# Optimization experiments

Measured on AMD Instinct MI355X. Metric: run time of the kernel, lower is better.

The kernel has to match this reference:

```python
import jax, jax.numpy as jnp
import numpy as np

IMG = 512
STRIDE = 16
K = 9
FM = IMG // STRIDE          # 32
N = FM * FM * K             # 9216 anchors
IOU_THR = 0.7
POST_NMS_TOPK = 300
C_FEAT = 512


def _conv(x, w, b, stride=1, padding='SAME'):
    y = jax.lax.conv_general_dilated(x, w, (stride, stride), padding,
                                     dimension_numbers=('NCHW', 'OIHW', 'NCHW'))
    return y + b[None, :, None, None]


def _make_anchors():
    scales = [64.0, 128.0, 256.0]
    ratios = [0.5, 1.0, 2.0]
    wh = np.array([[s * np.sqrt(r), s / np.sqrt(r)] for s in scales for r in ratios],
                  np.float32)                                    # [K,2]
    ctr = (np.arange(FM, dtype=np.float32) + 0.5) * STRIDE
    cy, cx = np.meshgrid(ctr, ctr, indexing='ij')               # [FM,FM]
    c = np.stack([cx, cy], -1)[:, :, None, :]                   # [FM,FM,1,2]
    half = wh[None, None, :, :] / 2.0                           # [1,1,K,2]
    boxes = np.concatenate([c - half, c + half], -1)            # [FM,FM,K,4]
    return boxes.reshape(-1, 4)


def setup_inputs():
    key = jax.random.key(0)
    ks = jax.random.split(key, 5)
    p = lambda k, shp, s: jax.random.normal(k, shp, jnp.float32) * s
    return {
        'input_image': jax.random.normal(ks[0], (1, 3, IMG, IMG), jnp.float32),
        'anchors': jnp.asarray(_make_anchors()),
        'w_bb': p(ks[1], (C_FEAT, 3, STRIDE, STRIDE), 0.05),
        'b_bb': jnp.zeros((C_FEAT,), jnp.float32),
        'w_rpn': p(ks[2], (C_FEAT, C_FEAT, 3, 3), 0.02),
        'b_rpn': jnp.zeros((C_FEAT,), jnp.float32),
        'w_cls': p(ks[3], (2 * K, C_FEAT, 1, 1), 0.01),
        'b_cls': jnp.zeros((2 * K,), jnp.float32),
        'w_box': p(ks[4], (4 * K, C_FEAT, 1, 1), 0.01),
        'b_box': jnp.zeros((4 * K,), jnp.float32),
    }


def _decode_clip(anchors, deltas):
    # apply_delta_to_anchors + clip_boxes
    wa = anchors[:, 2] - anchors[:, 0]
    ha = anchors[:, 3] - anchors[:, 1]
    cxa = anchors[:, 0] + 0.5 * wa
    cya = anchors[:, 1] + 0.5 * ha
    dx, dy = deltas[:, 0], deltas[:, 1]
    dw = jnp.clip(deltas[:, 2], -4.0, 4.0)   # numeric guard on exp
    dh = jnp.clip(deltas[:, 3], -4.0, 4.0)
    cx = cxa + dx * wa
    cy = cya + dy * ha
    w = wa * jnp.exp(dw)
    h = ha * jnp.exp(dh)
    x1 = jnp.maximum(cx - 0.5 * w, 0.0)
    y1 = jnp.maximum(cy - 0.5 * h, 0.0)
    x2 = jnp.minimum(cx + 0.5 * w, IMG - 1.0)
    y2 = jnp.minimum(cy + 0.5 * h, IMG - 1.0)
    return jnp.stack([x1, y1, x2, y2], -1)


def _iou_matrix(b):
    x1, y1, x2, y2 = b[:, 0], b[:, 1], b[:, 2], b[:, 3]
    area = (x2 - x1) * (y2 - y1)
    iw = jnp.clip(jnp.minimum(x2[:, None], x2[None, :]) - jnp.maximum(x1[:, None], x1[None, :]), 0.0)
    ih = jnp.clip(jnp.minimum(y2[:, None], y2[None, :]) - jnp.maximum(y1[:, None], y1[None, :]), 0.0)
    inter = iw * ih
    return inter / (area[:, None] + area[None, :] - inter + 1e-9)


def _nms_keep(boxes_sorted):
    # boxes_sorted: [N,4] in descending score order; greedy hard NMS.
    iou = jax.lax.stop_gradient(_iou_matrix(boxes_sorted))  # [N,N]
    idx = jnp.arange(N)

    def body(i, keep):
        sup = keep[i] & (iou[i] > IOU_THR) & (idx > i)
        return keep & ~sup

    return jax.lax.fori_loop(0, N, body, jnp.ones((N,), bool))


def reference(input_image, anchors, w_bb, b_bb, w_rpn, b_rpn, w_cls, b_cls, w_box, b_box):
    # backbone
    feat = jax.nn.relu(_conv(input_image, w_bb, b_bb, stride=STRIDE, padding='VALID'))  # [1,512,32,32]
    # rpn
    hid = jax.nn.relu(_conv(feat, w_rpn, b_rpn))
    cls = _conv(hid, w_cls, b_cls)   # [1,2K,FM,FM]
    box = _conv(hid, w_box, b_box)   # [1,4K,FM,FM]
    # foreground scores: cls_scores[:, k:, :, :]
    scores = cls[0, K:, :, :].transpose(1, 2, 0).reshape(-1)                    # [N]
    deltas = box[0].reshape(K, 4, FM, FM).transpose(2, 3, 0, 1).reshape(-1, 4)  # [N,4]
    proposals = _decode_clip(anchors, deltas)
    order = jnp.argsort(-scores)
    boxes_s = proposals[order]
    keep = _nms_keep(boxes_s)
    # first 300 kept boxes (score order); fixed shape via stable argsort on keep flag
    sel = jnp.argsort((~keep).astype(jnp.int32), stable=True)[:POST_NMS_TOPK]
    return boxes_s[sel]
```

## Files before the change

kernel.cpp:

```cpp
#include <hip/hip_runtime.h>
#include <stdint.h>

typedef unsigned long long u64;

#define PTOT 1024
#define CF   512
#define NBOX 9216
#define NW   144
#define TOPK 300

__device__ __forceinline__ uint32_t score_key(float s) {
  uint32_t b = __float_as_uint(s);
  uint32_t o = (b & 0x80000000u) ? ~b : (b | 0x80000000u);
  return ~o;
}

#define FMA16() do { \
  acc[0][0] = fmaf(bv.x, av.x, acc[0][0]); \
  acc[0][1] = fmaf(bv.x, av.y, acc[0][1]); \
  acc[0][2] = fmaf(bv.x, av.z, acc[0][2]); \
  acc[0][3] = fmaf(bv.x, av.w, acc[0][3]); \
  acc[1][0] = fmaf(bv.y, av.x, acc[1][0]); \
  acc[1][1] = fmaf(bv.y, av.y, acc[1][1]); \
  acc[1][2] = fmaf(bv.y, av.z, acc[1][2]); \
  acc[1][3] = fmaf(bv.y, av.w, acc[1][3]); \
  acc[2][0] = fmaf(bv.z, av.x, acc[2][0]); \
  acc[2][1] = fmaf(bv.z, av.y, acc[2][1]); \
  acc[2][2] = fmaf(bv.z, av.z, acc[2][2]); \
  acc[2][3] = fmaf(bv.z, av.w, acc[2][3]); \
  acc[3][0] = fmaf(bv.w, av.x, acc[3][0]); \
  acc[3][1] = fmaf(bv.w, av.y, acc[3][1]); \
  acc[3][2] = fmaf(bv.w, av.z, acc[3][2]); \
  acc[3][3] = fmaf(bv.w, av.w, acc[3][3]); \
} while (0)

__global__ __launch_bounds__(256) void k_wt(const float* __restrict__ w_rpn,
                                            const float* __restrict__ w_bb,
                                            float* __restrict__ wT,
                                            float* __restrict__ wT1) {
  __shared__ float T[32][33];
  int bx = blockIdx.x;
  const float* src; float* dst; int K, kb;
  if (bx < 144) { src = w_rpn; dst = wT; K = 4608; kb = bx * 32; }
  else          { src = w_bb;  dst = wT1; K = 768; kb = (bx - 144) * 32; }
  const int cob = blockIdx.y * 32;
  const int tx = threadIdx.x & 31, ty = threadIdx.x >> 5;
#pragma unroll
  for (int r = 0; r < 32; r += 8)
    T[ty + r][tx] = src[(cob + ty + r) * K + kb + tx];
  __syncthreads();
#pragma unroll
  for (int r = 0; r < 32; r += 8)
    dst[(kb + ty + r) * 512 + cob + tx] = T[tx][ty + r];
}

__global__ __launch_bounds__(256) void k_conv1(const float* __restrict__ img,
                                               const float* __restrict__ wT1,
                                               float* __restrict__ featP) {
  __shared__ __align__(16) float As[32][72];
  __shared__ __align__(16) float Bs[32][64];
  const int t = threadIdx.x;
  const int pbase = blockIdx.x * 64;
  const int cobase = blockIdx.y * 64;
  const int z = blockIdx.z;
  const int pg = t & 15, cg = t >> 4;
  const int pp0 = pg * 4, cc0 = cg * 4;
  const int py0 = pbase >> 5;
  float acc[4][4] = {};
  for (int kb = 0; kb < 256; kb += 32) {
    const int ky0 = kb >> 4;
#pragma unroll
    for (int l0 = 0; l0 < 2048; l0 += 256) {
      int l = l0 + t;
      int seg = l >> 9, off = l & 511;
      int py_off = seg >> 1, ky_off = seg & 1;
      int row = (py0 + py_off) * 16 + ky0 + ky_off;
      float v = img[(z * 512 + row) * 512 + off];
      As[ky_off * 16 + (off & 15)][py_off * 32 + (off >> 4)] = v;
    }
#pragma unroll
    for (int it = 0; it < 2; ++it) {
      int idx4 = it * 256 + t;
      int k = idx4 >> 4, co4 = (idx4 & 15) << 2;
      *(float4*)&Bs[k][co4] =
          *(const float4*)&wT1[(z * 256 + kb + k) * 512 + cobase + co4];
    }
    __syncthreads();
#pragma unroll
    for (int kk = 0; kk < 32; ++kk) {
      float4 av = *(const float4*)&As[kk][pp0];
      float4 bv = *(const float4*)&Bs[kk][cc0];
      FMA16();
    }
    __syncthreads();
  }
#pragma unroll
  for (int i = 0; i < 4; ++i) {
    float* o = &featP[((size_t)z * CF + cobase + cc0 + i) * PTOT + pbase + pp0];
    *(float4*)o = make_float4(acc[i][0], acc[i][1], acc[i][2], acc[i][3]);
  }
}

__global__ __launch_bounds__(256) void k_reduce1(const float* __restrict__ featP,
                                                 const float* __restrict__ bias,
                                                 float* __restrict__ feat) {
  int idx4 = blockIdx.x * 256 + threadIdx.x;
  int co = idx4 >> 8;
  const float4* f = (const float4*)featP;
  float4 a = f[idx4];
  float4 b = f[idx4 + 131072];
  float4 c = f[idx4 + 262144];
  float bb = bias[co];
  float4 o;
  o.x = fmaxf(a.x + b.x + c.x + bb, 0.f);
  o.y = fmaxf(a.y + b.y + c.y + bb, 0.f);
  o.z = fmaxf(a.z + b.z + c.z + bb, 0.f);
  o.w = fmaxf(a.w + b.w + c.w + bb, 0.f);
  ((float4*)feat)[idx4] = o;
}

__global__ __launch_bounds__(256) void k_conv2(const float* __restrict__ feat,
                                               const float* __restrict__ wT,
                                               float* __restrict__ hidP,
                                               int ciPerZ) {
  __shared__ __align__(16) float As[8][6][44];
  __shared__ __align__(16) float Bs[72 * 64];
  const int t = threadIdx.x;
  const int pyb = blockIdx.x * 4;
  const int cob = blockIdx.y * 64;
  const int z = blockIdx.z;
  const int cib = z * ciPerZ;
  const int pg = t & 15, cg = t >> 4;
  const int prow = pg >> 2, px0 = (pg & 3) * 8;
  const int co0 = cg * 4;
  float acc[4][8] = {};
  for (int cc = 0; cc < ciPerZ; cc += 8) {
    {
      int idx4 = t;
#pragma unroll
      for (int it = 0; it < 2; ++it, idx4 += 256) {
        if (idx4 < 480) {
          int ci = idx4 / 60;
          int rem = idx4 - ci * 60;
          int row = rem / 10;
          int col4 = (rem - row * 10) << 2;
          int x = col4 - 4;
          int gy = pyb + row - 1;
          float4 v = make_float4(0.f, 0.f, 0.f, 0.f);
          if (x >= 0 && x < 32 && gy >= 0 && gy < 32)
            v = *(const float4*)&feat[(cib + cc + ci) * PTOT + gy * 32 + x];
          *(float4*)&As[ci][row][col4] = v;
        }
      }
    }
    {
      const int kg0 = (cib + cc) * 9;
      int idx4 = t;
#pragma unroll
      for (int it = 0; it < 5; ++it, idx4 += 256) {
        if (idx4 < 1152) {
          int k = idx4 >> 4;
          int co4 = (idx4 & 15) << 2;
          *(float4*)&Bs[k * 64 + co4] =
              *(const float4*)&wT[(kg0 + k) * 512 + cob + co4];
        }
      }
    }
    __syncthreads();
#pragma unroll 1
    for (int ci = 0; ci < 8; ++ci) {
#pragma unroll
      for (int dy = 0; dy < 3; ++dy) {
        const float* Ar = &As[ci][prow + dy][px0];
        float rw[16];
        *(float4*)&rw[0]  = *(const float4*)&Ar[0];
        *(float4*)&rw[4]  = *(const float4*)&Ar[4];
        *(float4*)&rw[8]  = *(const float4*)&Ar[8];
        *(float4*)&rw[12] = *(const float4*)&Ar[12];
#pragma unroll
        for (int dx = 0; dx < 3; ++dx) {
          const float* Bp = &Bs[(ci * 9 + dy * 3 + dx) * 64 + co0];
          float4 b0 = *(const float4*)&Bp[0];
          float bm[4] = {b0.x, b0.y, b0.z, b0.w};
#pragma unroll
          for (int m = 0; m < 4; ++m)
#pragma unroll
            for (int j = 0; j < 8; ++j)
              acc[m][j] = fmaf(rw[3 + dx + j], bm[m], acc[m][j]);
        }
      }
    }
    __syncthreads();
  }
  const int prowg = pyb + prow;
#pragma unroll
  for (int m = 0; m < 4; ++m) {
    int co = cob + co0 + m;
    float* o = &hidP[((size_t)z * CF + co) * PTOT + prowg * 32 + px0];
    *(float4*)&o[0] = make_float4(acc[m][0], acc[m][1], acc[m][2], acc[m][3]);
    *(float4*)&o[4] = make_float4(acc[m][4], acc[m][5], acc[m][6], acc[m][7]);
  }
}

__global__ __launch_bounds__(256) void k_reduce2(const float* __restrict__ hidP,
                                                 const float* __restrict__ bias,
                                                 float* __restrict__ hid_t, int Z) {
  __shared__ float T[64][65];
  const int co0 = blockIdx.x * 64, p0 = blockIdx.y * 64;
  const int t = threadIdx.x;
#pragma unroll
  for (int it = 0; it < 4; ++it) {
    int idx4 = it * 256 + t;
    int co = idx4 >> 4, p4 = (idx4 & 15) << 2;
    float4 s = make_float4(0.f, 0.f, 0.f, 0.f);
    for (int zz = 0; zz < Z; ++zz) {
      float4 v = *(const float4*)&hidP[((size_t)zz * CF + co0 + co) * PTOT + p0 + p4];
      s.x += v.x; s.y += v.y; s.z += v.z; s.w += v.w;
    }
    float b = bias[co0 + co];
    T[co][p4 + 0] = fmaxf(s.x + b, 0.f);
    T[co][p4 + 1] = fmaxf(s.y + b, 0.f);
    T[co][p4 + 2] = fmaxf(s.z + b, 0.f);
    T[co][p4 + 3] = fmaxf(s.w + b, 0.f);
  }
  __syncthreads();
#pragma unroll
  for (int it = 0; it < 4; ++it) {
    int idx4 = it * 256 + t;
    int p = idx4 >> 4, co4 = (idx4 & 15) << 2;
    float4 o = make_float4(T[co4][p], T[co4 + 1][p], T[co4 + 2][p], T[co4 + 3][p]);
    *(float4*)&hid_t[(size_t)(p0 + p) * CF + co0 + co4] = o;
  }
}

__global__ __launch_bounds__(256) void k_heads(const float* __restrict__ hid_t,
                                               const float* __restrict__ wcls,
                                               const float* __restrict__ bcls,
                                               const float* __restrict__ wbox,
                                               const float* __restrict__ bbox,
                                               float* __restrict__ scores,
                                               float* __restrict__ deltas) {
  const int t = threadIdx.x;
  const int lane = t & 63, w = t >> 6;
  const int p = blockIdx.x * 4 + w;
  const float* hp = &hid_t[(size_t)p * CF + lane * 8];
  float4 h0 = *(const float4*)hp;
  float4 h1 = *(const float4*)(hp + 4);
#pragma unroll 1
  for (int ch = 0; ch < 45; ++ch) {
    const float* wp = (ch < 9) ? &wcls[(9 + ch) * CF] : &wbox[(ch - 9) * CF];
    float4 w0 = *(const float4*)(wp + lane * 8);
    float4 w1 = *(const float4*)(wp + lane * 8 + 4);
    float s = h0.x * w0.x + h0.y * w0.y + h0.z * w0.z + h0.w * w0.w +
              h1.x * w1.x + h1.y * w1.y + h1.z * w1.z + h1.w * w1.w;
#pragma unroll
    for (int off = 32; off >= 1; off >>= 1) s += __shfl_xor(s, off, 64);
    if (lane == 0) {
      if (ch < 9) scores[p * 9 + ch] = s + bcls[9 + ch];
      else        deltas[p * 36 + (ch - 9)] = s + bbox[ch - 9];
    }
  }
}

__global__ __launch_bounds__(256) void k_decode(const float* __restrict__ deltas,
                                                const float* __restrict__ anchors,
                                                float4* __restrict__ props) {
  int n = blockIdx.x * 256 + threadIdx.x;
  float4 a = ((const float4*)anchors)[n];
  float4 d = ((const float4*)deltas)[n];
  float wa = a.z - a.x, ha = a.w - a.y;
  float cxa = a.x + 0.5f * wa, cya = a.y + 0.5f * ha;
  float dw = fminf(fmaxf(d.z, -4.f), 4.f);
  float dh = fminf(fmaxf(d.w, -4.f), 4.f);
  float cx = cxa + d.x * wa, cy = cya + d.y * ha;
  float ww = wa * expf(dw), hh = ha * expf(dh);
  float x1 = fmaxf(cx - 0.5f * ww, 0.f);
  float y1 = fmaxf(cy - 0.5f * hh, 0.f);
  float x2 = fminf(cx + 0.5f * ww, 511.f);
  float y2 = fminf(cy + 0.5f * hh, 511.f);
  props[n] = make_float4(x1, y1, x2, y2);
}

__global__ __launch_bounds__(1024) void k_sort1(const float* __restrict__ scores,
                                                u64* __restrict__ keys) {
  __shared__ u64 lds[8192];
  const int t = threadIdx.x;
  const int base = blockIdx.x * 8192;
  const bool desc = (blockIdx.x == 1);
#pragma unroll
  for (int l0 = 0; l0 < 8192; l0 += 1024) {
    int l = l0 + t, g = base + l;
    u64 kv = ~0ull;
    if (g < NBOX) kv = ((u64)score_key(scores[g]) << 32) | (u64)g;
    lds[l] = kv;
  }
  for (int k = 2; k <= 8192; k <<= 1) {
    for (int j = k >> 1; j > 0; j >>= 1) {
      __syncthreads();
#pragma unroll
      for (int m = 0; m < 4; ++m) {
        int pr = m * 1024 + t;
        int i = ((pr & ~(j - 1)) << 1) | (pr & (j - 1));
        int l2 = i | j;
        bool ascBlk = ((i & k) == 0);
        bool dirAsc = desc ? !ascBlk : ascBlk;
        u64 x = lds[i], y = lds[l2];
        bool sw = dirAsc ? (x > y) : (x < y);
        if (sw) { lds[i] = y; lds[l2] = x; }
      }
    }
  }
  __syncthreads();
#pragma unroll
  for (int l0 = 0; l0 < 8192; l0 += 1024) {
    int l = l0 + t;
    keys[base + l] = lds[l];
  }
}

__global__ __launch_bounds__(256) void k_sort2(u64* __restrict__ keys) {
  int i = blockIdx.x * 256 + threadIdx.x;
  u64 x = keys[i], y = keys[i + 8192];
  if (x > y) { keys[i] = y; keys[i + 8192] = x; }
}

__global__ __launch_bounds__(1024) void k_sort3(const u64* __restrict__ keys,
                                                const float4* __restrict__ props,
                                                float4* __restrict__ boxesS) {
  __shared__ u64 lds[8192];
  const int t = threadIdx.x;
  const int base = blockIdx.x * 8192;
#pragma unroll
  for (int l0 = 0; l0 < 8192; l0 += 1024) {
    int l = l0 + t;
    lds[l] = keys[base + l];
  }
  for (int j = 4096; j > 0; j >>= 1) {
    __syncthreads();
#pragma unroll
    for (int m = 0; m < 4; ++m) {
      int pr = m * 1024 + t;
      int i = ((pr & ~(j - 1)) << 1) | (pr & (j - 1));
      int l2 = i | j;
      u64 x = lds[i], y = lds[l2];
      if (x > y) { lds[i] = y; lds[l2] = x; }
    }
  }
  __syncthreads();
#pragma unroll
  for (int l0 = 0; l0 < 8192; l0 += 1024) {
    int l = l0 + t, g = base + l;
    if (g < NBOX) {
      int idx = (int)(lds[l] & 0xffffffffull);
      boxesS[g] = props[idx];
    }
  }
}

__global__ __launch_bounds__(256) void k_iou(const float4* __restrict__ boxesS,
                                             u64* __restrict__ mask) {
  __shared__ float4 cb[4][64];
  __shared__ float ca[4][64];
  const int t = threadIdx.x;
  const int lane = t & 63, w = t >> 6;
  const int u = blockIdx.x;
  const int v = blockIdx.y * 4 + w + 1;
  int y = u + v; if (y >= 145) y -= 145;
  const int a_ = min(u, y), b_ = max(u, y);
  const int iw = a_, wj = b_ - 1;

  {
    float4 c = boxesS[wj * 64 + lane];
    cb[w][lane] = c;
    ca[w][lane] = (c.z - c.x) * (c.w - c.y);
  }
  __syncthreads();

  const int i = iw * 64 + lane;
  float4 a = boxesS[i];
  float areaA = (a.z - a.x) * (a.w - a.y);
  u64 bits = 0;
#pragma unroll 4
  for (int jj = 0; jj < 64; ++jj) {
    int j = wj * 64 + jj;
    float4 c = cb[w][jj];
    float iw_ = fmaxf(fminf(a.z, c.z) - fmaxf(a.x, c.x), 0.f);
    float ih_ = fmaxf(fminf(a.w, c.w) - fmaxf(a.y, c.y), 0.f);
    float inter = iw_ * ih_;
    float uni = areaA + ca[w][jj] - inter + 1e-9f;
    float thr = 0.7f * uni;
    bool pos = uni > 0.f;
    bool sup = pos && (inter > thr);
    if (pos && (fabsf(inter - thr) <= thr * 1e-5f))
      sup = (inter / uni) > 0.7f;
    bits |= ((u64)(sup && (j > i))) << jj;
  }
  mask[(size_t)i * NW + wj] = bits;
}

__global__ __launch_bounds__(64) void k_scan(const u64* __restrict__ mask,
                                             const float4* __restrict__ boxesS,
                                             float* __restrict__ out) {
  __shared__ u64 Dbuf[64];
  __shared__ u64 keepArr[NW];
  __shared__ int pf[NW + 2];
  __shared__ int outIdx[TOPK];
  const int lane = threadIdx.x;

  u64 r0 = 0, r1 = 0, r2 = 0;
  int keptCount = 0;
  int stopSpan = NW - 1;

  u64 dcur = mask[(size_t)lane * NW];

  for (int wb = 0; wb < NW; ++wb) {
    Dbuf[lane] = dcur;
    __syncthreads();

    u64 v = (wb < 64) ? r0 : ((wb < 128) ? r1 : r2);
    u64 R = __shfl(v, wb & 63, 64);

    u64 dnext = 0;
    if (wb + 1 < NW)
      dnext = mask[(size_t)((wb + 1) * 64 + lane) * NW + (wb + 1)];

    u64 keepmask = 0;
    if (R != ~0ull) {
#pragma unroll
      for (int c = 0; c < 2; ++c) {
        u64 d[32];
#pragma unroll
        for (int r = 0; r < 32; ++r) d[r] = Dbuf[c * 32 + r];
#pragma unroll
        for (int r = 0; r < 32; ++r) {
          int rl = c * 32 + r;
          u64 keep = ((R >> rl) & 1ull) ^ 1ull;
          keepmask |= keep << rl;
          R |= d[r] & (0ull - keep);
        }
      }
      u64 km = keepmask;
      while (km) {
        int first = wb * 64 + __ffsll((long long)km) - 1;
        int idx[8];
#pragma unroll
        for (int s = 0; s < 8; ++s) {
          if (km) { idx[s] = wb * 64 + __ffsll((long long)km) - 1; km &= km - 1; }
          else    { idx[s] = first; }
        }
        u64 A[8], B[8], C[8];
#pragma unroll
        for (int s = 0; s < 8; ++s) {
          const u64* q = mask + (size_t)idx[s] * NW;
          A[s] = q[lane];
          B[s] = q[lane + 64];
          C[s] = (lane < 16) ? q[lane + 128] : 0ull;
        }
#pragma unroll
        for (int s = 0; s < 8; ++s) { r0 |= A[s]; r1 |= B[s]; r2 |= C[s]; }
      }
      keptCount += __popcll(keepmask);
    }
    if (lane == 0) keepArr[wb] = keepmask;
    dcur = dnext;
    if (keptCount >= TOPK) { stopSpan = wb; break; }
  }

  __syncthreads();
  if (lane == 0) {
    int acc = 0;
    for (int s = 0; s <= stopSpan; ++s) { pf[s] = acc; acc += __popcll(keepArr[s]); }
    pf[stopSpan + 1] = acc;
  }
  __syncthreads();
  const int keptTotal = pf[stopSpan + 1];

  for (int s = lane; s <= stopSpan; s += 64) {
    u64 km = keepArr[s];
    int slot = pf[s];
    while (km && slot < TOPK) {
      int rl = __ffsll((long long)km) - 1; km &= km - 1;
      outIdx[slot++] = s * 64 + rl;
    }
  }
  if (keptTotal < TOPK) {
    for (int s = lane; s <= stopSpan; s += 64) {
      u64 rm = ~keepArr[s];
      int slot = keptTotal + s * 64 - pf[s];
      while (rm && slot < TOPK) {
        int rl = __ffsll((long long)rm) - 1; rm &= rm - 1;
        outIdx[slot++] = s * 64 + rl;
      }
    }
  }
  __syncthreads();
#pragma unroll
  for (int k0 = 0; k0 < TOPK + 63; k0 += 64) {
    int k = k0 + lane;
    if (k < TOPK) {
      float4 bx = boxesS[outIdx[k]];
      out[k * 4 + 0] = bx.x;
      out[k * 4 + 1] = bx.y;
      out[k * 4 + 2] = bx.z;
      out[k * 4 + 3] = bx.w;
    }
  }
}

extern "C" void kernel_launch(void* const* d_in, const int* in_sizes, int n_in,
                              void* d_out, int out_size, void* d_ws, size_t ws_size,
                              hipStream_t stream) {
  const float* img   = (const float*)d_in[0];
  const float* anch  = (const float*)d_in[1];
  const float* w_bb  = (const float*)d_in[2];
  const float* b_bb  = (const float*)d_in[3];
  const float* w_rpn = (const float*)d_in[4];
  const float* b_rpn = (const float*)d_in[5];
  const float* w_cls = (const float*)d_in[6];
  const float* b_cls = (const float*)d_in[7];
  const float* w_box = (const float*)d_in[8];
  const float* b_box = (const float*)d_in[9];

  char* ws = (char*)d_ws;
  int Z = 16;
  if (ws_size < 22806528ull + 16ull * 2097152ull) Z = 8;
  if (ws_size < 22806528ull + 8ull * 2097152ull)  Z = 4;
  if (ws_size < 22806528ull + 4ull * 2097152ull)  Z = 2;
  if (ws_size < 22806528ull + 2ull * 2097152ull)  Z = 1;

  float* wT    = (float*)(ws);
  float* wT1   = (float*)(ws + 9437184);
  float* featP = (float*)(ws + 11010048);
  float* feat  = (float*)(ws + 17301504);
  float* hidP  = (float*)(ws + 19398656);
  char*  hte   = ws + 19398656 + (size_t)Z * 2097152;
  float* hid_t = (float*)hte;
  char*  tail  = hte + 2097152;
  float*  scores = (float*)(tail);
  float*  deltas = (float*)(tail + 0x40000);
  float4* props  = (float4*)(tail + 0x80000);
  u64*    keys   = (u64*)(tail + 0xC0000);
  float4* boxesS = (float4*)(tail + 0x100000);
  u64*    mask   = (u64*)(ws + 11010048);
  float*  out    = (float*)d_out;

  hipLaunchKernelGGL(k_wt, dim3(168, 16), dim3(256), 0, stream, w_rpn, w_bb, wT, wT1);
  hipLaunchKernelGGL(k_conv1, dim3(16, 8, 3), dim3(256), 0, stream, img, wT1, featP);
  hipLaunchKernelGGL(k_reduce1, dim3(512), dim3(256), 0, stream, featP, b_bb, feat);
  hipLaunchKernelGGL(k_conv2, dim3(8, 8, Z), dim3(256), 0, stream, feat, wT, hidP, 512 / Z);
  hipLaunchKernelGGL(k_reduce2, dim3(8, 16), dim3(256), 0, stream, hidP, b_rpn, hid_t, Z);
  hipLaunchKernelGGL(k_heads, dim3(256), dim3(256), 0, stream, hid_t, w_cls, b_cls, w_box, b_box, scores, deltas);
  hipLaunchKernelGGL(k_decode, dim3(36), dim3(256), 0, stream, deltas, anch, props);
  hipLaunchKernelGGL(k_sort1, dim3(2), dim3(1024), 0, stream, scores, keys);
  hipLaunchKernelGGL(k_sort2, dim3(32), dim3(256), 0, stream, keys);
  hipLaunchKernelGGL(k_sort3, dim3(2), dim3(1024), 0, stream, keys, props, boxesS);
  hipLaunchKernelGGL(k_iou, dim3(145, 18), dim3(256), 0, stream, boxesS, mask);
  hipLaunchKernelGGL(k_scan, dim3(1), dim3(64), 0, stream, mask, boxesS, out);
}
```

Baseline: 376.2 us.

## Prefetch conv2 tiles into registers and fuse decode and merge into sort

The conv2 loop now loads the next channel chunk of input and weights into registers while the current chunk is being computed from shared memory, hiding global load latency behind the FMAs. Separately, the box decode kernel and the cross-half bitonic merge kernel are removed. Their work is folded into k_sort3, which does the min/max merge while loading keys and decodes boxes on the gathered index. This cuts two launches and a props round-trip through memory, at the cost of more registers in conv2, which may lower occupancy.

```diff
diff --git a/kernel.cpp b/kernel.cpp
--- a/kernel.cpp
+++ b/kernel.cpp
@@ -133,40 +133,67 @@
   const int pg = t & 15, cg = t >> 4;
   const int prow = pg >> 2, px0 = (pg & 3) * 8;
   const int co0 = cg * 4;
+
+  int a_ci0, a_row0, a_col40, a_off0; bool a_val0, a_in0;
+  int a_ci1, a_row1, a_col41, a_off1; bool a_val1, a_in1;
+  {
+    int idx4 = t;
+    a_val0 = idx4 < 480;
+    int ci = idx4 / 60, rem = idx4 - ci * 60, row = rem / 10;
+    int col4 = (rem - row * 10) << 2;
+    int x = col4 - 4, gy = pyb + row - 1;
+    a_in0 = a_val0 && x >= 0 && x < 32 && gy >= 0 && gy < 32;
+    a_ci0 = ci; a_row0 = row; a_col40 = col4;
+    a_off0 = ci * PTOT + gy * 32 + x;
+  }
+  {
+    int idx4 = 256 + t;
+    a_val1 = idx4 < 480;
+    int ci = idx4 / 60, rem = idx4 - ci * 60, row = rem / 10;
+    int col4 = (rem - row * 10) << 2;
+    int x = col4 - 4, gy = pyb + row - 1;
+    a_in1 = a_val1 && x >= 0 && x < 32 && gy >= 0 && gy < 32;
+    a_ci1 = ci; a_row1 = row; a_col41 = col4;
+    a_off1 = ci * PTOT + gy * 32 + x;
+  }
+  int b_k[5], b_co4[5]; bool b_val[5];
+#pragma unroll
+  for (int it = 0; it < 5; ++it) {
+    int idx4 = it * 256 + t;
+    b_val[it] = idx4 < 1152;
+    b_k[it] = idx4 >> 4; b_co4[it] = (idx4 & 15) << 2;
+  }
+
+  float4 pa0 = make_float4(0.f,0.f,0.f,0.f), pa1 = pa0;
+  float4 pb[5];
+#pragma unroll
+  for (int s = 0; s < 5; ++s) pb[s] = make_float4(0.f,0.f,0.f,0.f);
+
+#define PREFETCH(CC) do {                                                       \
+    const float* fbase = feat + (size_t)(cib + (CC)) * PTOT;                    \
+    if (a_in0) pa0 = *(const float4*)&fbase[a_off0];                            \
+    if (a_in1) pa1 = *(const float4*)&fbase[a_off1];                            \
+    const float* wbase = wT + ((size_t)(cib + (CC)) * 9) * 512 + cob;           \
+    _Pragma("unroll")                                                           \
+    for (int s = 0; s < 5; ++s)                                                 \
+      if (b_val[s]) pb[s] = *(const float4*)&wbase[(size_t)b_k[s] * 512 + b_co4[s]]; \
+  } while (0)
+
+  PREFETCH(0);
+
   float acc[4][8] = {};
   for (int cc = 0; cc < ciPerZ; cc += 8) {
-    {
-      int idx4 = t;
-#pragma unroll
-      for (int it = 0; it < 2; ++it, idx4 += 256) {
-        if (idx4 < 480) {
-          int ci = idx4 / 60;
-          int rem = idx4 - ci * 60;
-          int row = rem / 10;
-          int col4 = (rem - row * 10) << 2;
-          int x = col4 - 4;
-          int gy = pyb + row - 1;
-          float4 v = make_float4(0.f, 0.f, 0.f, 0.f);
-          if (x >= 0 && x < 32 && gy >= 0 && gy < 32)
-            v = *(const float4*)&feat[(cib + cc + ci) * PTOT + gy * 32 + x];
-          *(float4*)&As[ci][row][col4] = v;
-        }
-      }
-    }
-    {
-      const int kg0 = (cib + cc) * 9;
-      int idx4 = t;
-#pragma unroll
-      for (int it = 0; it < 5; ++it, idx4 += 256) {
-        if (idx4 < 1152) {
-          int k = idx4 >> 4;
-          int co4 = (idx4 & 15) << 2;
-          *(float4*)&Bs[k * 64 + co4] =
-              *(const float4*)&wT[(kg0 + k) * 512 + cob + co4];
-        }
-      }
-    }
+    if (a_val0) *(float4*)&As[a_ci0][a_row0][a_col40] =
+        a_in0 ? pa0 : make_float4(0.f,0.f,0.f,0.f);
+    if (a_val1) *(float4*)&As[a_ci1][a_row1][a_col41] =
+        a_in1 ? pa1 : make_float4(0.f,0.f,0.f,0.f);
+#pragma unroll
+    for (int s = 0; s < 5; ++s)
+      if (b_val[s]) *(float4*)&Bs[b_k[s] * 64 + b_co4[s]] = pb[s];
     __syncthreads();
+
+    if (cc + 8 < ciPerZ) PREFETCH(cc + 8);
+
 #pragma unroll 1
     for (int ci = 0; ci < 8; ++ci) {
 #pragma unroll
@@ -192,6 +219,7 @@
     }
     __syncthreads();
   }
+#undef PREFETCH
   const int prowg = pyb + prow;
 #pragma unroll
   for (int m = 0; m < 4; ++m) {
@@ -262,25 +290,6 @@
   }
 }
 
-__global__ __launch_bounds__(256) void k_decode(const float* __restrict__ deltas,
-                                                const float* __restrict__ anchors,
-                                                float4* __restrict__ props) {
-  int n = blockIdx.x * 256 + threadIdx.x;
-  float4 a = ((const float4*)anchors)[n];
-  float4 d = ((const float4*)deltas)[n];
-  float wa = a.z - a.x, ha = a.w - a.y;
-  float cxa = a.x + 0.5f * wa, cya = a.y + 0.5f * ha;
-  float dw = fminf(fmaxf(d.z, -4.f), 4.f);
-  float dh = fminf(fmaxf(d.w, -4.f), 4.f);
-  float cx = cxa + d.x * wa, cy = cya + d.y * ha;
-  float ww = wa * expf(dw), hh = ha * expf(dh);
-  float x1 = fmaxf(cx - 0.5f * ww, 0.f);
-  float y1 = fmaxf(cy - 0.5f * hh, 0.f);
-  float x2 = fminf(cx + 0.5f * ww, 511.f);
-  float y2 = fminf(cy + 0.5f * hh, 511.f);
-  props[n] = make_float4(x1, y1, x2, y2);
-}
-
 __global__ __launch_bounds__(1024) void k_sort1(const float* __restrict__ scores,
                                                 u64* __restrict__ keys) {
   __shared__ u64 lds[8192];
@@ -318,22 +327,19 @@
   }
 }
 
-__global__ __launch_bounds__(256) void k_sort2(u64* __restrict__ keys) {
-  int i = blockIdx.x * 256 + threadIdx.x;
-  u64 x = keys[i], y = keys[i + 8192];
-  if (x > y) { keys[i] = y; keys[i + 8192] = x; }
-}
-
 __global__ __launch_bounds__(1024) void k_sort3(const u64* __restrict__ keys,
-                                                const float4* __restrict__ props,
+                                                const float* __restrict__ anchors,
+                                                const float* __restrict__ deltas,
                                                 float4* __restrict__ boxesS) {
   __shared__ u64 lds[8192];
   const int t = threadIdx.x;
-  const int base = blockIdx.x * 8192;
+  const int b = blockIdx.x;
+  const int base = b * 8192;
 #pragma unroll
   for (int l0 = 0; l0 < 8192; l0 += 1024) {
     int l = l0 + t;
-    lds[l] = keys[base + l];
+    u64 x = keys[l], y = keys[l + 8192];
+    lds[l] = b ? (x > y ? x : y) : (x > y ? y : x);
   }
   for (int j = 4096; j > 0; j >>= 1) {
     __syncthreads();
@@ -352,7 +358,19 @@
     int l = l0 + t, g = base + l;
     if (g < NBOX) {
       int idx = (int)(lds[l] & 0xffffffffull);
-      boxesS[g] = props[idx];
+      float4 a = ((const float4*)anchors)[idx];
+      float4 d = ((const float4*)deltas)[idx];
+      float wa = a.z - a.x, ha = a.w - a.y;
+      float cxa = a.x + 0.5f * wa, cya = a.y + 0.5f * ha;
+      float dw = fminf(fmaxf(d.z, -4.f), 4.f);
+      float dh = fminf(fmaxf(d.w, -4.f), 4.f);
+      float cx = cxa + d.x * wa, cy = cya + d.y * ha;
+      float ww = wa * expf(dw), hh = ha * expf(dh);
+      float x1 = fmaxf(cx - 0.5f * ww, 0.f);
+      float y1 = fmaxf(cy - 0.5f * hh, 0.f);
+      float x2 = fminf(cx + 0.5f * ww, 511.f);
+      float y2 = fminf(cy + 0.5f * hh, 511.f);
+      boxesS[g] = make_float4(x1, y1, x2, y2);
     }
   }
 }
@@ -538,7 +556,6 @@
   char*  tail  = hte + 2097152;
   float*  scores = (float*)(tail);
   float*  deltas = (float*)(tail + 0x40000);
-  float4* props  = (float4*)(tail + 0x80000);
   u64*    keys   = (u64*)(tail + 0xC0000);
   float4* boxesS = (float4*)(tail + 0x100000);
   u64*    mask   = (u64*)(ws + 11010048);
@@ -550,10 +567,8 @@
   hipLaunchKernelGGL(k_conv2, dim3(8, 8, Z), dim3(256), 0, stream, feat, wT, hidP, 512 / Z);
   hipLaunchKernelGGL(k_reduce2, dim3(8, 16), dim3(256), 0, stream, hidP, b_rpn, hid_t, Z);
   hipLaunchKernelGGL(k_heads, dim3(256), dim3(256), 0, stream, hid_t, w_cls, b_cls, w_box, b_box, scores, deltas);
-  hipLaunchKernelGGL(k_decode, dim3(36), dim3(256), 0, stream, deltas, anch, props);
   hipLaunchKernelGGL(k_sort1, dim3(2), dim3(1024), 0, stream, scores, keys);
-  hipLaunchKernelGGL(k_sort2, dim3(32), dim3(256), 0, stream, keys);
-  hipLaunchKernelGGL(k_sort3, dim3(2), dim3(1024), 0, stream, keys, props, boxesS);
+  hipLaunchKernelGGL(k_sort3, dim3(2), dim3(1024), 0, stream, keys, anch, deltas, boxesS);
   hipLaunchKernelGGL(k_iou, dim3(145, 18), dim3(256), 0, stream, boxesS, mask);
   hipLaunchKernelGGL(k_scan, dim3(1), dim3(64), 0, stream, mask, boxesS, out);
 }
```

New measurement: 384.5 us. 2.2% more time.
